# Kernel optimization log

Measured on AMD Instinct MI355X. Metric: run time of the kernel, lower is better.

Reference implementation:

```python
import jax, jax.numpy as jnp
import numpy as np

D_MODEL = 1024
N_HEADS = 16
D_HEAD = D_MODEL // N_HEADS
D_FF = 4096
B, T = 2, 2048


def setup_inputs() -> dict:
    key = jax.random.key(0)
    ks = jax.random.split(key, 8)
    s = 0.02
    return {
        "x": jax.random.normal(ks[0], (B, T, D_MODEL), dtype=jnp.float32),
        "wq": jax.random.normal(ks[1], (D_MODEL, D_MODEL), dtype=jnp.float32) * s,
        "wk": jax.random.normal(ks[2], (D_MODEL, D_MODEL), dtype=jnp.float32) * s,
        "wv": jax.random.normal(ks[3], (D_MODEL, D_MODEL), dtype=jnp.float32) * s,
        "wo": jax.random.normal(ks[4], (D_MODEL, D_MODEL), dtype=jnp.float32) * s,
        "w1": jax.random.normal(ks[5], (D_FF, D_MODEL), dtype=jnp.float32) * s,
        "b1": jnp.zeros((D_FF,), dtype=jnp.float32),
        "w2": jax.random.normal(ks[6], (D_MODEL, D_FF), dtype=jnp.float32) * s,
        "b2": jnp.zeros((D_MODEL,), dtype=jnp.float32),
        "ln1_g": jnp.ones((D_MODEL,), dtype=jnp.float32),
        "ln1_b": jnp.zeros((D_MODEL,), dtype=jnp.float32),
        "ln2_g": jnp.ones((D_MODEL,), dtype=jnp.float32),
        "ln2_b": jnp.zeros((D_MODEL,), dtype=jnp.float32),
    }


def _layernorm(x, g, b, eps=1e-5):
    mu = jnp.mean(x, axis=-1, keepdims=True)
    var = jnp.mean(jnp.square(x - mu), axis=-1, keepdims=True)
    return (x - mu) * jax.lax.rsqrt(var + eps) * g + b


def reference(x, wq, wk, wv, wo, w1, b1, w2, b2, ln1_g, ln1_b, ln2_g, ln2_b):
    Bsz, Tlen, C = x.shape
    h = _layernorm(x, ln1_g, ln1_b)
    # torch Linear: y = h @ W^T ; reshape to [B, H, T, Dh]
    def proj(w):
        return (h @ w.T).reshape(Bsz, Tlen, N_HEADS, D_HEAD).transpose(0, 2, 1, 3)
    q, k, v = proj(wq), proj(wk), proj(wv)
    scores = jnp.einsum('bhqd,bhkd->bhqk', q, k) / np.sqrt(D_HEAD).astype(np.float32)
    p = jax.nn.softmax(scores.astype(jnp.float32), axis=-1).astype(scores.dtype)
    out = jnp.einsum('bhqk,bhkd->bhqd', p, v)
    out = out.transpose(0, 2, 1, 3).reshape(Bsz, Tlen, C)
    x = x + out @ wo.T
    h2 = _layernorm(x, ln2_g, ln2_b)
    ff = jax.nn.gelu(h2 @ w1.T + b1, approximate=False) @ w2.T + b2
    return x + ff
```

## Files before the change

kernel.cpp:

```cpp
#include <hip/hip_runtime.h>
#include <hip/hip_bf16.h>
#include <math.h>

#define DM   1024
#define NH   16
#define DH   64
#define DFF  4096
#define BB   2
#define TT   2048
#define MTOK (BB*TT)
#define QS   3072

typedef unsigned short u16;
typedef unsigned int   u32;
typedef __attribute__((ext_vector_type(8))) __bf16 bf16x8;
typedef __attribute__((ext_vector_type(4))) float  f32x4;

__device__ inline float bf2f(u16 u) { return __uint_as_float(((u32)u) << 16); }
__device__ inline u16 f2bf(float f) {
  u32 u = __float_as_uint(f);
  u += 0x7FFFu + ((u >> 16) & 1u);
  return (u16)(u >> 16);
}
__device__ inline u32 packtrunc(float lo, float hi) {
  return __builtin_amdgcn_perm(__float_as_uint(hi), __float_as_uint(lo), 0x07060302u);
}
__device__ inline float fexp2(float x) { return __builtin_amdgcn_exp2f(x); }

__device__ inline void gload_lds16(const void* g, void* l) {
  __builtin_amdgcn_global_load_lds(
      (const __attribute__((address_space(1))) void*)g,
      (__attribute__((address_space(3))) void*)l,
      16, 0, 0);
}

__global__ __launch_bounds__(256) void prep(
    const float* __restrict__ wq, const float* __restrict__ wk, const float* __restrict__ wv,
    const float* __restrict__ wo, const float* __restrict__ w1, const float* __restrict__ w2,
    const float* __restrict__ x, const float* __restrict__ g, const float* __restrict__ be,
    u16* __restrict__ wqkv_b, u16* __restrict__ wo_b, u16* __restrict__ w1_b,
    u16* __restrict__ w2_b, u16* __restrict__ h1)
{
  const int blk = blockIdx.x;
  if (blk < 12288) {
    const float* src; u16* dst; int idx;
    if (blk < 3072) {
      idx = blk * 256 + threadIdx.x;
      const int sel = idx >> 18;
      const int j = idx & 0x3FFFF;
      src = sel == 0 ? wq : (sel == 1 ? wk : wv);
      dst = wqkv_b;
      float4 v = ((const float4*)src)[j];
      ushort4 o; o.x = f2bf(v.x); o.y = f2bf(v.y); o.z = f2bf(v.z); o.w = f2bf(v.w);
      ((ushort4*)dst)[idx] = o;
      return;
    } else if (blk < 4096) { src = wo; dst = wo_b; idx = (blk - 3072) * 256 + threadIdx.x; }
    else if (blk < 8192)   { src = w1; dst = w1_b; idx = (blk - 4096) * 256 + threadIdx.x; }
    else                   { src = w2; dst = w2_b; idx = (blk - 8192) * 256 + threadIdx.x; }
    float4 v = ((const float4*)src)[idx];
    ushort4 o; o.x = f2bf(v.x); o.y = f2bf(v.y); o.z = f2bf(v.z); o.w = f2bf(v.w);
    ((ushort4*)dst)[idx] = o;
    return;
  }
  const int w = threadIdx.x >> 6, lane = threadIdx.x & 63;
  const int row = (blk - 12288) * 4 + w;
  const float4* xr = (const float4*)(x + (size_t)row * DM);
  float4 v[4];
  float s = 0.f, s2 = 0.f;
#pragma unroll
  for (int i = 0; i < 4; i++) {
    v[i] = xr[i * 64 + lane];
    s  += v[i].x + v[i].y + v[i].z + v[i].w;
    s2 += v[i].x * v[i].x + v[i].y * v[i].y + v[i].z * v[i].z + v[i].w * v[i].w;
  }
#pragma unroll
  for (int off = 32; off > 0; off >>= 1) {
    s  += __shfl_xor(s,  off);
    s2 += __shfl_xor(s2, off);
  }
  const float mu = s * (1.f / DM);
  const float rs = rsqrtf(s2 * (1.f / DM) - mu * mu + 1e-5f);
  u16* orow = h1 + (size_t)row * DM;
#pragma unroll
  for (int i = 0; i < 4; i++) {
    const float4 gg = ((const float4*)g)[i * 64 + lane];
    const float4 bb = ((const float4*)be)[i * 64 + lane];
    ushort4 o;
    o.x = f2bf((v[i].x - mu) * rs * gg.x + bb.x);
    o.y = f2bf((v[i].y - mu) * rs * gg.y + bb.y);
    o.z = f2bf((v[i].z - mu) * rs * gg.z + bb.z);
    o.w = f2bf((v[i].w - mu) * rs * gg.w + bb.w);
    ((ushort4*)orow)[i * 64 + lane] = o;
  }
}

__global__ __launch_bounds__(256) void reduce_ln(
    const float* __restrict__ x, const float* __restrict__ P,
    const float* __restrict__ g, const float* __restrict__ be,
    float* __restrict__ xmid, u16* __restrict__ h2)
{
  const float* P0 = P;
  const float* P1 = P + (size_t)MTOK * DM;
  const int w = threadIdx.x >> 6, lane = threadIdx.x & 63;
  const int row = blockIdx.x * 4 + w;
  const size_t roff = (size_t)row * DM;
  float4 v[4];
  float s = 0.f, s2 = 0.f;
#pragma unroll
  for (int i = 0; i < 4; i++) {
    const float4 a = ((const float4*)(x  + roff))[i * 64 + lane];
    const float4 p = ((const float4*)(P0 + roff))[i * 64 + lane];
    const float4 qv = ((const float4*)(P1 + roff))[i * 64 + lane];
    v[i].x = a.x + p.x + qv.x; v[i].y = a.y + p.y + qv.y;
    v[i].z = a.z + p.z + qv.z; v[i].w = a.w + p.w + qv.w;
    ((float4*)(xmid + roff))[i * 64 + lane] = v[i];
    s  += v[i].x + v[i].y + v[i].z + v[i].w;
    s2 += v[i].x * v[i].x + v[i].y * v[i].y + v[i].z * v[i].z + v[i].w * v[i].w;
  }
#pragma unroll
  for (int off = 32; off > 0; off >>= 1) {
    s  += __shfl_xor(s,  off);
    s2 += __shfl_xor(s2, off);
  }
  const float mu = s * (1.f / DM);
  const float rs = rsqrtf(s2 * (1.f / DM) - mu * mu + 1e-5f);
  u16* orow = h2 + roff;
#pragma unroll
  for (int i = 0; i < 4; i++) {
    const float4 gg = ((const float4*)g)[i * 64 + lane];
    const float4 bb = ((const float4*)be)[i * 64 + lane];
    ushort4 o;
    o.x = f2bf((v[i].x - mu) * rs * gg.x + bb.x);
    o.y = f2bf((v[i].y - mu) * rs * gg.y + bb.y);
    o.z = f2bf((v[i].z - mu) * rs * gg.z + bb.z);
    o.w = f2bf((v[i].w - mu) * rs * gg.w + bb.w);
    ((ushort4*)orow)[i * 64 + lane] = o;
  }
}

__global__ __launch_bounds__(256) void reduce_out(
    const float* __restrict__ Q, const float* __restrict__ xmid,
    const float* __restrict__ b2, float* __restrict__ out)
{
  const float* Q0 = Q;
  const float* Q1 = Q + (size_t)MTOK * DM;
  const int i = blockIdx.x * 256 + threadIdx.x;
  const float4 a = ((const float4*)xmid)[i];
  const float4 p = ((const float4*)Q0)[i];
  const float4 qv = ((const float4*)Q1)[i];
  const float4 bb = ((const float4*)b2)[i & (DM / 4 - 1)];
  float4 o;
  o.x = a.x + p.x + qv.x + bb.x; o.y = a.y + p.y + qv.y + bb.y;
  o.z = a.z + p.z + qv.z + bb.z; o.w = a.w + p.w + qv.w + bb.w;
  ((float4*)out)[i] = o;
}

template <int EPI, int BN>
__global__ __launch_bounds__(256) void gemm_bt(
    const u16* __restrict__ A, const u16* __restrict__ Bw,
    int M, int N, int K,
    const float* __restrict__ bias,
    u16* __restrict__ outB, float oscale, int scaleN)
{
  constexpr int NJ = BN / 32;
  __shared__ u16 As[128 * 64];
  __shared__ u16 Bs[BN * 64];

  const int tid  = threadIdx.x;
  const int w    = tid >> 6;
  const int lane = tid & 63;
  const int wr   = w >> 1, wc = w & 1;
  const int q    = lane >> 4;
  const int li   = lane & 15;
  const int rowBase = blockIdx.y * 128;
  const int colBase = blockIdx.x * BN;

  const int lr = lane >> 3;
  const int cs = (lane & 7) ^ lr;
  const u16* Abase = A  + (size_t)(rowBase + lr) * K + cs * 8;
  const u16* Bbase = Bw + (size_t)(colBase + lr) * K + cs * 8;

  f32x4 acc[4][NJ] = {};

  for (int k0 = 0; k0 < K; k0 += 64) {
    __syncthreads();
#pragma unroll
    for (int jj = 0; jj < 4; jj++) {
      const int rb = (w * 4 + jj) * 8;
      gload_lds16(Abase + (size_t)rb * K + k0, &As[rb * 64]);
    }
#pragma unroll
    for (int jj = 0; jj < NJ; jj++) {
      const int rb = (w * NJ + jj) * 8;
      gload_lds16(Bbase + (size_t)rb * K + k0, &Bs[rb * 64]);
    }
    __syncthreads();
#pragma unroll
    for (int kk = 0; kk < 2; kk++) {
      bf16x8 fa[4], fb[NJ];
      const int pos = (kk * 4 + q) ^ (li & 7);
#pragma unroll
      for (int i = 0; i < 4; i++) {
        const int row = wr * 64 + i * 16 + li;
        fa[i] = *(const bf16x8*)&As[row * 64 + pos * 8];
      }
#pragma unroll
      for (int j = 0; j < NJ; j++) {
        const int row = wc * (BN / 2) + j * 16 + li;
        fb[j] = *(const bf16x8*)&Bs[row * 64 + pos * 8];
      }
#pragma unroll
      for (int i = 0; i < 4; i++)
#pragma unroll
        for (int j = 0; j < NJ; j++)
          acc[i][j] = __builtin_amdgcn_mfma_f32_16x16x32_bf16(fa[i], fb[j], acc[i][j], 0, 0, 0);
    }
  }

#pragma unroll
  for (int i = 0; i < 4; i++) {
#pragma unroll
    for (int j = 0; j < NJ; j++) {
      const int col = colBase + wc * (BN / 2) + j * 16 + li;
      float bv = 0.f;
      if constexpr (EPI == 2) bv = bias[col];
#pragma unroll
      for (int r = 0; r < 4; r++) {
        const int row = rowBase + wr * 64 + i * 16 + q * 4 + r;
        float v = acc[i][j][r] + bv;
        if constexpr (EPI == 2) {
          const float z = fexp2(-v * (2.302213f + 0.1029625f * v * v));
          v = v * __builtin_amdgcn_rcpf(1.f + z);
        }
        if constexpr (EPI == 0) {
          const float sc = (col < scaleN) ? oscale : 1.f;
          v *= sc;
        }
        outB[(size_t)row * N + col] = f2bf(v);
      }
    }
  }
}

template <int EPI>
__global__ __launch_bounds__(512, 2) void gemm256(
    const u16* __restrict__ A, const u16* __restrict__ Bw,
    int M, int N, int K,
    const float* __restrict__ bias,
    u16* __restrict__ outB, float oscale, int scaleN)
{
  __shared__ u16 lds[3 * 16384];

  const int tid  = threadIdx.x;
  const int w    = tid >> 6;
  const int lane = tid & 63;
  const int wr   = w >> 2, wc = w & 3;
  const int q    = lane >> 4, li = lane & 15;

  const int nbx = gridDim.x, nwg = nbx * gridDim.y;
  int bid = blockIdx.y * nbx + blockIdx.x;
  bid = (bid & 7) * (nwg >> 3) + (bid >> 3);
  const int bx = bid % nbx, by = bid / nbx;
  const int rowBase = by * 256, colBase = bx * 256;

  const int srow = lane >> 2;
  const int schk = (lane & 3) ^ ((lane >> 3) & 3);
  const u16* Asrc = A  + (size_t)(rowBase + srow) * K + schk * 8;
  const u16* Bsrc = Bw + (size_t)(colBase + srow) * K + schk * 8;
  const int wbase = w * 16;

  auto stage = [&](int kt, int bsel) {
    const int k0 = kt * 32;
    u16* bb = &lds[bsel * 16384];
#pragma unroll
    for (int half = 0; half < 2; half++) {
      const int rb = half * 128 + wbase;
      gload_lds16(Asrc + (size_t)rb * K + k0, &bb[rb * 32]);
      gload_lds16(Bsrc + (size_t)rb * K + k0, &bb[8192 + rb * 32]);
    }
  };

  f32x4 acc[8][4] = {};
  const int NT = K >> 5;
  const int pos = q ^ ((li >> 1) & 3);

  stage(0, 0);
  stage(1, 1);

  int csel = 0, ssel = 2;
  for (int kt = 0; kt < NT; ++kt) {
    if (kt < NT - 1) asm volatile("s_waitcnt vmcnt(4)" ::: "memory");
    else             asm volatile("s_waitcnt vmcnt(0)" ::: "memory");
    __builtin_amdgcn_s_barrier();
    const u16* bb = &lds[csel * 16384];
    bf16x8 fa[8], fb[4];
#pragma unroll
    for (int m = 0; m < 8; m++)
      fa[m] = *(const bf16x8*)&bb[(wr * 128 + m * 16 + li) * 32 + pos * 8];
#pragma unroll
    for (int n = 0; n < 4; n++)
      fb[n] = *(const bf16x8*)&bb[8192 + (wc * 64 + n * 16 + li) * 32 + pos * 8];
    if (kt + 2 < NT) stage(kt + 2, ssel);
    __builtin_amdgcn_s_setprio(1);
#pragma unroll
    for (int m = 0; m < 8; m++)
#pragma unroll
      for (int n = 0; n < 4; n++)
        acc[m][n] = __builtin_amdgcn_mfma_f32_16x16x32_bf16(fa[m], fb[n], acc[m][n], 0, 0, 0);
    __builtin_amdgcn_s_setprio(0);
    csel = (csel == 2) ? 0 : csel + 1;
    ssel = (ssel == 2) ? 0 : ssel + 1;
  }

#pragma unroll
  for (int n = 0; n < 4; n++) {
    const int col = colBase + wc * 64 + n * 16 + li;
    float bv = 0.f;
    if constexpr (EPI == 2) bv = bias[col];
#pragma unroll
    for (int m = 0; m < 8; m++) {
#pragma unroll
      for (int r = 0; r < 4; r++) {
        const int row = rowBase + wr * 128 + m * 16 + q * 4 + r;
        float v = acc[m][n][r] + bv;
        if constexpr (EPI == 2) {
          const float z = fexp2(-v * (2.302213f + 0.1029625f * v * v));
          v = v * __builtin_amdgcn_rcpf(1.f + z);
        }
        if constexpr (EPI == 0) {
          const float sc = (col < scaleN) ? oscale : 1.f;
          v *= sc;
        }
        outB[(size_t)row * N + col] = f2bf(v);
      }
    }
  }
}

__global__ __launch_bounds__(256) void gemm_sk(
    const u16* __restrict__ A, const u16* __restrict__ Bw,
    int N, int K, int KLEN, float* __restrict__ P)
{
  __shared__ u16 As[128 * 64];
  __shared__ u16 Bs[64 * 64];

  const int tid  = threadIdx.x;
  const int w    = tid >> 6;
  const int lane = tid & 63;
  const int wr   = w >> 1, wc = w & 1;
  const int q    = lane >> 4;
  const int li   = lane & 15;
  const int rowBase = blockIdx.y * 128;
  const int colBase = blockIdx.x * 64;
  const int koff = blockIdx.z * KLEN;

  const int lr = lane >> 3;
  const int cs = (lane & 7) ^ lr;
  const u16* Abase = A  + (size_t)(rowBase + lr) * K + koff + cs * 8;
  const u16* Bbase = Bw + (size_t)(colBase + lr) * K + koff + cs * 8;

  f32x4 acc[4][2] = {};

  for (int k0 = 0; k0 < KLEN; k0 += 64) {
    __syncthreads();
#pragma unroll
    for (int jj = 0; jj < 4; jj++) {
      const int rb = (w * 4 + jj) * 8;
      gload_lds16(Abase + (size_t)rb * K + k0, &As[rb * 64]);
    }
#pragma unroll
    for (int jj = 0; jj < 2; jj++) {
      const int rb = (w * 2 + jj) * 8;
      gload_lds16(Bbase + (size_t)rb * K + k0, &Bs[rb * 64]);
    }
    __syncthreads();
#pragma unroll
    for (int kk = 0; kk < 2; kk++) {
      bf16x8 fa[4], fb[2];
      const int pos = (kk * 4 + q) ^ (li & 7);
#pragma unroll
      for (int i = 0; i < 4; i++) {
        const int row = wr * 64 + i * 16 + li;
        fa[i] = *(const bf16x8*)&As[row * 64 + pos * 8];
      }
#pragma unroll
      for (int j = 0; j < 2; j++) {
        const int row = wc * 32 + j * 16 + li;
        fb[j] = *(const bf16x8*)&Bs[row * 64 + pos * 8];
      }
#pragma unroll
      for (int i = 0; i < 4; i++)
#pragma unroll
        for (int j = 0; j < 2; j++)
          acc[i][j] = __builtin_amdgcn_mfma_f32_16x16x32_bf16(fa[i], fb[j], acc[i][j], 0, 0, 0);
    }
  }

  float* Pz = P + (size_t)blockIdx.z * MTOK * DM;
#pragma unroll
  for (int i = 0; i < 4; i++)
#pragma unroll
    for (int j = 0; j < 2; j++) {
      const int col = colBase + wc * 32 + j * 16 + li;
#pragma unroll
      for (int r = 0; r < 4; r++) {
        const int row = rowBase + wr * 64 + i * 16 + q * 4 + r;
        Pz[(size_t)row * N + col] = acc[i][j][r];
      }
    }
}

__global__ __launch_bounds__(256) void transpose_v(
    const u16* __restrict__ vq, u16* __restrict__ vt)
{
  __shared__ u16 t[64][72];
  const int bh = blockIdx.x, b = bh >> 4, h = bh & 15;
  const int t0 = blockIdx.y * 64;
  const int tid = threadIdx.x;
  const int r = tid >> 2, c = (tid & 3) * 16;
  const u16* src = vq + (size_t)(b * TT + t0 + r) * QS + h * DH + c;
#pragma unroll
  for (int i = 0; i < 4; i++)
    *(ushort4*)&t[r][c + i * 4] = ((const ushort4*)src)[i];
  __syncthreads();
  const int dh = tid >> 2, tt = (tid & 3) * 16;
  u16* dst = vt + ((size_t)bh * 64 + dh) * TT + t0 + tt;
#pragma unroll
  for (int i = 0; i < 4; i++) {
    ushort4 o;
    o.x = t[tt + i * 4 + 0][dh]; o.y = t[tt + i * 4 + 1][dh];
    o.z = t[tt + i * 4 + 2][dh]; o.w = t[tt + i * 4 + 3][dh];
    ((ushort4*)dst)[i] = o;
  }
}

__global__ __launch_bounds__(512) void attn_mfma(
    const u16* __restrict__ qb, const u16* __restrict__ kb,
    const u16* __restrict__ vt, u16* __restrict__ ob)
{
  __shared__ u16 Ks[2][64 * 64];
  __shared__ u16 Vs[2][64 * 64];
  __shared__ u16 Sh[8 * 16 * 72];

  const int tid = threadIdx.x, w = tid >> 6, lane = tid & 63;
  const int q = lane >> 4, li = lane & 15;
  const int bh = blockIdx.x, b = bh >> 4, h = bh & 15;
  const int q0 = blockIdx.y * 128;
  const int lr8 = lane >> 3, lc8 = lane & 7;

#pragma unroll
  for (int jj = 0; jj < 2; jj++) {
    const int rb = w * 16 + jj * 8;
    const int row = rb + lr8;
    const int cs = lc8 ^ (row & 7);
    gload_lds16(qb + (size_t)(b * TT + q0 + row) * QS + h * DH + cs * 8,
                &Sh[rb * 64]);
  }
  __syncthreads();

  bf16x8 qf[2];
#pragma unroll
  for (int kk = 0; kk < 2; kk++) {
    const int row = w * 16 + li;
    const int pos = (kk * 4 + q) ^ (li & 7);
    qf[kk] = *(const bf16x8*)&Sh[row * 64 + pos * 8];
  }

  auto stage = [&](int buf, int kt) {
    const int rb = w * 8;
    const int row = rb + lr8;
    const int cs = lc8 ^ (row & 7);
    gload_lds16(kb + (size_t)(b * TT + kt + row) * QS + h * DH + cs * 8,
                &Ks[buf][rb * 64]);
    gload_lds16(vt + ((size_t)bh * 64 + row) * TT + kt + cs * 8,
                &Vs[buf][rb * 64]);
  };

  f32x4 ot[4] = {};
  float lsum = 0.f;
  u16* Pw = &Sh[w * 16 * 72];

  stage(0, 0);
  for (int it = 0; it < TT / 64; it++) {
    __syncthreads();
    if (it + 1 < TT / 64) stage((it + 1) & 1, (it + 1) * 64);
    const u16* Kc = Ks[it & 1];
    const u16* Vc = Vs[it & 1];

    f32x4 st[4] = {};
#pragma unroll
    for (int kk = 0; kk < 2; kk++)
#pragma unroll
      for (int i = 0; i < 4; i++) {
        const int pos = (kk * 4 + q) ^ (li & 7);
        const bf16x8 kf = *(const bf16x8*)&Kc[(i * 16 + li) * 64 + pos * 8];
        st[i] = __builtin_amdgcn_mfma_f32_16x16x32_bf16(kf, qf[kk], st[i], 0, 0, 0);
      }

    u32 pk[4][2];
#pragma unroll
    for (int i = 0; i < 4; i++) {
      const float p0 = fexp2(st[i][0]);
      const float p1 = fexp2(st[i][1]);
      const float p2 = fexp2(st[i][2]);
      const float p3 = fexp2(st[i][3]);
      lsum += (p0 + p1) + (p2 + p3);
      pk[i][0] = packtrunc(p0, p1);
      pk[i][1] = packtrunc(p2, p3);
    }

#pragma unroll
    for (int i = 0; i < 4; i++) {
      const int a = li * 72 + i * 16 + q * 4;
      *(u32*)&Pw[a]     = pk[i][0];
      *(u32*)&Pw[a + 2] = pk[i][1];
    }

#pragma unroll
    for (int kk = 0; kk < 2; kk++) {
      const bf16x8 pf = *(const bf16x8*)&Pw[li * 72 + kk * 32 + q * 8];
#pragma unroll
      for (int m = 0; m < 4; m++) {
        const int pos = (kk * 4 + q) ^ (li & 7);
        const bf16x8 vf = *(const bf16x8*)&Vc[(m * 16 + li) * 64 + pos * 8];
        ot[m] = __builtin_amdgcn_mfma_f32_16x16x32_bf16(vf, pf, ot[m], 0, 0, 0);
      }
    }
  }

  float s = lsum;
  s += __shfl_xor(s, 16);
  s += __shfl_xor(s, 32);
  const float inv = 1.f / s;
#pragma unroll
  for (int m = 0; m < 4; m++) {
    const int a = li * 72 + m * 16 + q * 4;
    *(u32*)&Pw[a]     = packtrunc(ot[m][0] * inv, ot[m][1] * inv);
    *(u32*)&Pw[a + 2] = packtrunc(ot[m][2] * inv, ot[m][3] * inv);
  }
#pragma unroll
  for (int pass = 0; pass < 2; pass++) {
    const int row = pass * 8 + lr8;
    const bf16x8 v = *(const bf16x8*)&Pw[row * 72 + lc8 * 8];
    const int token = q0 + w * 16 + row;
    *(bf16x8*)(ob + ((size_t)(b * TT + token) * NH + h) * DH + lc8 * 8) = v;
  }
}

extern "C" void kernel_launch(void* const* d_in, const int* in_sizes, int n_in,
                              void* d_out, int out_size, void* d_ws, size_t ws_size,
                              hipStream_t stream) {
  const float* x    = (const float*)d_in[0];
  const float* wq   = (const float*)d_in[1];
  const float* wk   = (const float*)d_in[2];
  const float* wv   = (const float*)d_in[3];
  const float* wo   = (const float*)d_in[4];
  const float* w1   = (const float*)d_in[5];
  const float* b1   = (const float*)d_in[6];
  const float* w2   = (const float*)d_in[7];
  const float* b2   = (const float*)d_in[8];
  const float* ln1g = (const float*)d_in[9];
  const float* ln1b = (const float*)d_in[10];
  const float* ln2g = (const float*)d_in[11];
  const float* ln2b = (const float*)d_in[12];

  size_t off = 0;
  char* base = (char*)d_ws;
  auto alloc = [&](size_t bytes) { void* p = base + off; off += bytes; return p; };

  u16* wqkv_b = (u16*)alloc((size_t)3 * DM * DM * 2);
  u16* wo_b   = (u16*)alloc((size_t)DM * DM * 2);
  u16* w1_b   = (u16*)alloc((size_t)DFF * DM * 2);
  u16* w2_b   = (u16*)alloc((size_t)DM * DFF * 2);
  u16* h1     = (u16*)alloc((size_t)MTOK * DM * 2);
  u16* qkvb   = (u16*)alloc((size_t)MTOK * QS * 2);
  u16* attn   = (u16*)alloc((size_t)MTOK * DM * 2);
  u16* h2     = (u16*)alloc((size_t)MTOK * DM * 2);
  u16* ff1    = (u16*)alloc((size_t)MTOK * DFF * 2);
  float* xmid = (float*)alloc((size_t)MTOK * DM * 4);
  u16* vtb    = ff1;
  float* woP  = (float*)ff1;
  float* ff2P = (float*)h1;
  (void)ws_size; (void)in_sizes; (void)n_in; (void)out_size;

  prep<<<13312, 256, 0, stream>>>(wq, wk, wv, wo, w1, w2, x, ln1g, ln1b,
                                  wqkv_b, wo_b, w1_b, w2_b, h1);

  const float QSCALE = 0.125f * 1.44269504088896340736f;
  gemm_bt<0, 128><<<dim3(QS / 128, MTOK / 128), 256, 0, stream>>>(
      h1, wqkv_b, MTOK, QS, DM, nullptr, qkvb, QSCALE, DM);

  transpose_v<<<dim3(BB * NH, TT / 64), 256, 0, stream>>>(qkvb + 2 * DM, vtb);
  attn_mfma<<<dim3(BB * NH, TT / 128), 512, 0, stream>>>(qkvb, qkvb + DM, vtb, attn);

  gemm_sk<<<dim3(DM / 64, MTOK / 128, 2), 256, 0, stream>>>(
      attn, wo_b, DM, DM, DM / 2, woP);
  reduce_ln<<<MTOK / 4, 256, 0, stream>>>(x, woP, ln2g, ln2b, xmid, h2);

  gemm256<2><<<dim3(DFF / 256, MTOK / 256), 512, 0, stream>>>(
      h2, w1_b, MTOK, DFF, DM, b1, ff1, 1.f, 0);
  gemm_sk<<<dim3(DM / 64, MTOK / 128, 2), 256, 0, stream>>>(
      ff1, w2_b, DM, DFF, DFF / 2, ff2P);
  reduce_out<<<MTOK * DM / 4 / 256, 256, 0, stream>>>(ff2P, xmid, b2, (float*)d_out);
}
```

Baseline: 337.0 us.

## Deepen FF1 GEMM pipeline to 4 LDS stages with split A/B staging

The FF1 GEMM (gemm256) now uses four LDS buffers instead of three, prefetching three K-tiles ahead. Each K step is split into two halves, with the A and B tile loads issued separately and interleaved with the two MFMA halves. K is made a template constant, and the block-to-tile mapping is changed to 4x4 supertiles per XCD to improve L2 locality. The deeper pipeline targets global load latency, but the extra barriers per step and the larger LDS footprint may reduce occupancy or add synchronization overhead.

```diff
diff --git a/kernel.cpp b/kernel.cpp
--- a/kernel.cpp
+++ b/kernel.cpp
@@ -242,14 +242,16 @@
   }
 }
 
-template <int EPI>
+template <int EPI, int KC>
 __global__ __launch_bounds__(512, 2) void gemm256(
     const u16* __restrict__ A, const u16* __restrict__ Bw,
-    int M, int N, int K,
+    int N,
     const float* __restrict__ bias,
     u16* __restrict__ outB, float oscale, int scaleN)
 {
-  __shared__ u16 lds[3 * 16384];
+  constexpr int K  = KC;
+  constexpr int NT = KC / 32;
+  __shared__ u16 lds[4 * 16384];
 
   const int tid  = threadIdx.x;
   const int w    = tid >> 6;
@@ -257,59 +259,85 @@
   const int wr   = w >> 2, wc = w & 3;
   const int q    = lane >> 4, li = lane & 15;
 
-  const int nbx = gridDim.x, nwg = nbx * gridDim.y;
-  int bid = blockIdx.y * nbx + blockIdx.x;
-  bid = (bid & 7) * (nwg >> 3) + (bid >> 3);
-  const int bx = bid % nbx, by = bid / nbx;
+  const int nbx = gridDim.x;
+  const int o   = blockIdx.y * nbx + blockIdx.x;
+  const int xcd = o & 7, i_x = o >> 3;
+  const int nsx = nbx >> 2;
+  const int super = xcd + 8 * (i_x >> 4);
+  const int wi  = i_x & 15;
+  const int bx  = (super % nsx) * 4 + (wi & 3);
+  const int by  = (super / nsx) * 4 + (wi >> 2);
   const int rowBase = by * 256, colBase = bx * 256;
 
   const int srow = lane >> 2;
   const int schk = (lane & 3) ^ ((lane >> 3) & 3);
   const u16* Asrc = A  + (size_t)(rowBase + srow) * K + schk * 8;
   const u16* Bsrc = Bw + (size_t)(colBase + srow) * K + schk * 8;
-  const int wbase = w * 16;
-
-  auto stage = [&](int kt, int bsel) {
+
+  auto stageA = [&](int kt, int bsel) {
     const int k0 = kt * 32;
-    u16* bb = &lds[bsel * 16384];
-#pragma unroll
-    for (int half = 0; half < 2; half++) {
-      const int rb = half * 128 + wbase;
-      gload_lds16(Asrc + (size_t)rb * K + k0, &bb[rb * 32]);
-      gload_lds16(Bsrc + (size_t)rb * K + k0, &bb[8192 + rb * 32]);
+    u16* dst = &lds[bsel * 16384];
+#pragma unroll
+    for (int j = 0; j < 2; j++) {
+      const int rb = w * 32 + j * 16;
+      gload_lds16(Asrc + (size_t)rb * K + k0, &dst[rb * 32]);
     }
   };
+  auto stageB = [&](int kt, int bsel) {
+    const int k0 = kt * 32;
+    u16* dst = &lds[bsel * 16384 + 8192];
+#pragma unroll
+    for (int j = 0; j < 2; j++) {
+      const int rb = w * 32 + j * 16;
+      gload_lds16(Bsrc + (size_t)rb * K + k0, &dst[rb * 32]);
+    }
+  };
 
   f32x4 acc[8][4] = {};
-  const int NT = K >> 5;
   const int pos = q ^ ((li >> 1) & 3);
 
-  stage(0, 0);
-  stage(1, 1);
-
-  int csel = 0, ssel = 2;
-  for (int kt = 0; kt < NT; ++kt) {
-    if (kt < NT - 1) asm volatile("s_waitcnt vmcnt(4)" ::: "memory");
-    else             asm volatile("s_waitcnt vmcnt(0)" ::: "memory");
+  stageA(0, 0); stageB(0, 0);
+  stageA(1, 1); stageB(1, 1);
+  stageA(2, 2); stageB(2, 2);
+
+  for (int t = 0; t < NT; ++t) {
+    if (t < NT - 2)      asm volatile("s_waitcnt vmcnt(8)" ::: "memory");
+    else if (t == NT - 2) asm volatile("s_waitcnt vmcnt(4)" ::: "memory");
+    else                 asm volatile("s_waitcnt vmcnt(0)" ::: "memory");
     __builtin_amdgcn_s_barrier();
-    const u16* bb = &lds[csel * 16384];
-    bf16x8 fa[8], fb[4];
-#pragma unroll
-    for (int m = 0; m < 8; m++)
+
+    const u16* bb = &lds[(t & 3) * 16384];
+    bf16x8 fa[4], fb[4];
+
+#pragma unroll
+    for (int m = 0; m < 4; m++)
       fa[m] = *(const bf16x8*)&bb[(wr * 128 + m * 16 + li) * 32 + pos * 8];
 #pragma unroll
     for (int n = 0; n < 4; n++)
       fb[n] = *(const bf16x8*)&bb[8192 + (wc * 64 + n * 16 + li) * 32 + pos * 8];
-    if (kt + 2 < NT) stage(kt + 2, ssel);
+    if (t + 3 < NT) stageA(t + 3, (t + 3) & 3);
+    __builtin_amdgcn_s_barrier();
     __builtin_amdgcn_s_setprio(1);
 #pragma unroll
-    for (int m = 0; m < 8; m++)
+    for (int m = 0; m < 4; m++)
 #pragma unroll
       for (int n = 0; n < 4; n++)
         acc[m][n] = __builtin_amdgcn_mfma_f32_16x16x32_bf16(fa[m], fb[n], acc[m][n], 0, 0, 0);
     __builtin_amdgcn_s_setprio(0);
-    csel = (csel == 2) ? 0 : csel + 1;
-    ssel = (ssel == 2) ? 0 : ssel + 1;
+    __builtin_amdgcn_s_barrier();
+
+#pragma unroll
+    for (int m = 0; m < 4; m++)
+      fa[m] = *(const bf16x8*)&bb[(wr * 128 + 64 + m * 16 + li) * 32 + pos * 8];
+    if (t + 3 < NT) stageB(t + 3, (t + 3) & 3);
+    __builtin_amdgcn_s_barrier();
+    __builtin_amdgcn_s_setprio(1);
+#pragma unroll
+    for (int m = 0; m < 4; m++)
+#pragma unroll
+      for (int n = 0; n < 4; n++)
+        acc[4 + m][n] = __builtin_amdgcn_mfma_f32_16x16x32_bf16(fa[m], fb[n], acc[4 + m][n], 0, 0, 0);
+    __builtin_amdgcn_s_setprio(0);
   }
 
 #pragma unroll
@@ -597,8 +625,8 @@
       attn, wo_b, DM, DM, DM / 2, woP);
   reduce_ln<<<MTOK / 4, 256, 0, stream>>>(x, woP, ln2g, ln2b, xmid, h2);
 
-  gemm256<2><<<dim3(DFF / 256, MTOK / 256), 512, 0, stream>>>(
-      h2, w1_b, MTOK, DFF, DM, b1, ff1, 1.f, 0);
+  gemm256<2, DM><<<dim3(DFF / 256, MTOK / 256), 512, 0, stream>>>(
+      h2, w1_b, DFF, b1, ff1, 1.f, 0);
   gemm_sk<<<dim3(DM / 64, MTOK / 128, 2), 256, 0, stream>>>(
       ff1, w2_b, DM, DFF, DFF / 2, ff2P);
   reduce_out<<<MTOK * DM / 4 / 256, 256, 0, stream>>>(ff2P, xmid, b2, (float*)d_out);
```

Result: no change. 335.2 us (-0.5%).
